# Kernel tuning notes

Hardware: AMD Instinct MI355X
Metric: run time of the kernel (lower is better)

Reference implementation:

```python
import jax, jax.numpy as jnp
import numpy as np

B, S, D, H = 4, 1024, 1024, 16
DH = D // H  # head_dim = 64


def setup_inputs() -> dict:
    key = jax.random.key(0)
    kq, kk, kv, kl, kwq, kwk, kwv, kwo = jax.random.split(key, 8)
    query = jax.random.normal(kq, (B, S, D), dtype=jnp.float32)
    key_t = jax.random.normal(kk, (B, S, D), dtype=jnp.float32)
    value = jax.random.normal(kv, (B, S, D), dtype=jnp.float32)
    # padding: keys at positions >= valid length are padded (True)
    lengths = jax.random.randint(kl, (B,), S // 2, S + 1)
    key_padding_mask = jnp.arange(S)[None, :] >= lengths[:, None]  # [B,S] bool
    scale = 1.0 / np.sqrt(D)
    Wq = jax.random.normal(kwq, (D, D), dtype=jnp.float32) * scale
    Wk = jax.random.normal(kwk, (D, D), dtype=jnp.float32) * scale
    Wv = jax.random.normal(kwv, (D, D), dtype=jnp.float32) * scale
    Wo = jax.random.normal(kwo, (D, D), dtype=jnp.float32) * scale
    gamma = jnp.ones((H,), dtype=jnp.float32)
    return {"query": query, "key": key_t, "value": value,
            "key_padding_mask": key_padding_mask,
            "Wq": Wq, "Wk": Wk, "Wv": Wv, "Wo": Wo, "gamma": gamma}


def reference(query, key, value, key_padding_mask, Wq, Wk, Wv, Wo, gamma):
    # nn.Linear(x) = x @ W.T (bias=False)
    q = jnp.einsum('bsd,ed->bse', query, Wq).reshape(B, S, H, DH).transpose(0, 2, 1, 3)  # [B,H,S,Dh]
    k = jnp.einsum('bsd,ed->bse', key, Wk).reshape(B, S, H, DH).transpose(0, 2, 1, 3)
    v = jnp.einsum('bsd,ed->bse', value, Wv).reshape(B, S, H, DH).transpose(0, 2, 1, 3)
    scores = jnp.einsum('bhqd,bhkd->bhqk', q, k) / jnp.sqrt(jnp.float32(DH))
    pad = key_padding_mask[:, None, None, :]  # [B,1,1,S]
    scores = jnp.where(pad, -jnp.inf, scores)
    v = jnp.where(key_padding_mask[:, None, :, None], 0.0, v)
    attn = jax.nn.softmax(scores, axis=-1)  # dropout p=0 (eval) -> identity
    ws = jnp.einsum('bhqk,bhkd->bhqd', attn, v)
    ws = ws * gamma[None, :, None, None]  # per-head scale
    ws = ws.transpose(0, 2, 1, 3).reshape(B, S, D)
    return jnp.einsum('bsd,ed->bse', ws, Wo)
```

## Files before the change

### kernel.cpp

```cpp
#include <hip/hip_runtime.h>
#include <math.h>

#define S_LEN 1024
#define DMODEL 1024

typedef __attribute__((ext_vector_type(8))) short bf16x8;
typedef __attribute__((ext_vector_type(4))) short bf16x4;
typedef __attribute__((ext_vector_type(4))) float f32x4;

#define MFMA16(a, b, c) __builtin_amdgcn_mfma_f32_16x16x32_bf16(a, b, c, 0, 0, 0)

#define WP (1024u * 1024u)
#define XP (4u * 1024u * 1024u)

__device__ __forceinline__ unsigned short rne_bf16(float f) {
    unsigned u = __float_as_uint(f);
    u += 0x7FFFu + ((u >> 16) & 1u);
    return (unsigned short)(u >> 16);
}

__device__ __forceinline__ void split_rne(float f, unsigned short& h, unsigned short& l) {
    unsigned short hh = rne_bf16(f);
    float lf = f - __uint_as_float(((unsigned)hh) << 16);
    h = hh;
    l = rne_bf16(lf);
}

typedef const __attribute__((address_space(1))) unsigned int* gas_t;
typedef __attribute__((address_space(3))) unsigned int* las_t;
__device__ __forceinline__ void glds16(const void* g, void* l) {
    __builtin_amdgcn_global_load_lds((gas_t)g, (las_t)l, 16, 0, 0);
}

__global__ __launch_bounds__(256)
void convert_wx(const float* __restrict__ W0, const float* __restrict__ W1,
                const float* __restrict__ W2, const float* __restrict__ W3,
                const float* __restrict__ Xq, const float* __restrict__ Xk,
                const float* __restrict__ Xv,
                unsigned short* __restrict__ Wpl, unsigned short* __restrict__ Xbase) {
    int blk = blockIdx.x;
    if (blk < 4096) {
        const int which = blk >> 10;
        const float* W = which == 0 ? W0 : which == 1 ? W1 : which == 2 ? W2 : W3;
        int i = ((blk & 1023) * 256 + threadIdx.x) * 4;
        float4 f = *(const float4*)&W[i];
        if (which == 3) {
            unsigned short* hi = Wpl + 3 * WP;
            unsigned short* lo = Wpl + 4 * WP;
            bf16x4 h, l;
            unsigned short hh, ll;
            split_rne(f.x, hh, ll); h[0] = (short)hh; l[0] = (short)ll;
            split_rne(f.y, hh, ll); h[1] = (short)hh; l[1] = (short)ll;
            split_rne(f.z, hh, ll); h[2] = (short)hh; l[2] = (short)ll;
            split_rne(f.w, hh, ll); h[3] = (short)hh; l[3] = (short)ll;
            *(bf16x4*)&hi[i] = h;
            *(bf16x4*)&lo[i] = l;
        } else {
            unsigned short* hi = Wpl + (size_t)which * WP;
            bf16x4 h;
            h[0] = (short)rne_bf16(f.x);
            h[1] = (short)rne_bf16(f.y);
            h[2] = (short)rne_bf16(f.z);
            h[3] = (short)rne_bf16(f.w);
            *(bf16x4*)&hi[i] = h;
        }
    } else {
        blk -= 4096;
        const int which = blk >> 12;
        const float* X = which == 0 ? Xq : which == 1 ? Xk : Xv;
        unsigned short* Xr = Xbase + (size_t)which * XP;
        int i = ((blk & 4095) * 256 + threadIdx.x) * 4;
        float4 f = *(const float4*)&X[i];
        bf16x4 h;
        h[0] = (short)rne_bf16(f.x);
        h[1] = (short)rne_bf16(f.y);
        h[2] = (short)rne_bf16(f.z);
        h[3] = (short)rne_bf16(f.w);
        *(bf16x4*)&Xr[i] = h;
    }
}

__global__ __launch_bounds__(256)
void gemm_proj(const unsigned short* __restrict__ Xbase,
               const unsigned short* __restrict__ Wpl,
               unsigned short* __restrict__ Obase) {
    __shared__ unsigned short AS[128 * 32];
    __shared__ unsigned short BS[128 * 32];

    const int z = blockIdx.z;
    const unsigned short* A = Xbase + (size_t)z * XP;
    const unsigned short* B = Wpl + (size_t)z * WP;

    const int t = threadIdx.x, lane = t & 63, w = t >> 6;
    const int quad = lane >> 4, l15 = lane & 15;
    const int wr = w & 1, wc = w >> 1;

    const int linb = blockIdx.x + (blockIdx.y << 3);
    const int swz = ((linb & 7) << 5) + (linb >> 3);
    const int bx = swz & 7, by = swz >> 3;
    const int rowBase = by * 128, colBase = bx * 128;

    const unsigned short* gA[2];
    const unsigned short* gB[2];
    unsigned short* lA[2];
    unsigned short* lB[2];
    #pragma unroll
    for (int e = 0; e < 2; e++) {
        int row = w * 32 + e * 16 + (lane >> 2);
        int cg = (lane & 3) ^ ((row >> 1) & 3);
        gA[e] = A + (size_t)(rowBase + row) * 1024 + cg * 8;
        gB[e] = B + (size_t)(colBase + row) * 1024 + cg * 8;
        lA[e] = &AS[(w * 32 + e * 16) * 32];
        lB[e] = &BS[(w * 32 + e * 16) * 32];
    }

    int aAd[4], bAd[4];
    #pragma unroll
    for (int i = 0; i < 4; i++) {
        int ra = wr * 64 + i * 16 + l15;
        aAd[i] = ra * 32 + (quad ^ ((ra >> 1) & 3)) * 8;
        int rb = wc * 64 + i * 16 + l15;
        bAd[i] = rb * 32 + (quad ^ ((rb >> 1) & 3)) * 8;
    }

    f32x4 acc[4][4] = {};

    for (int kt = 0; kt < 32; kt++) {
        if (kt) __syncthreads();
        const int ko = kt * 32;
        glds16(gA[0] + ko, lA[0]);
        glds16(gA[1] + ko, lA[1]);
        glds16(gB[0] + ko, lB[0]);
        glds16(gB[1] + ko, lB[1]);
        __syncthreads();

        bf16x8 af[4], bfr[4];
        #pragma unroll
        for (int i = 0; i < 4; i++) af[i] = *(const bf16x8*)&AS[aAd[i]];
        #pragma unroll
        for (int j = 0; j < 4; j++) bfr[j] = *(const bf16x8*)&BS[bAd[j]];
        #pragma unroll
        for (int j = 0; j < 4; j++)
            #pragma unroll
            for (int i = 0; i < 4; i++)
                acc[i][j] = MFMA16(af[i], bfr[j], acc[i][j]);
    }

    unsigned short* O = Obase + (size_t)z * XP;
    #pragma unroll
    for (int i = 0; i < 4; i++)
        #pragma unroll
        for (int j = 0; j < 4; j++)
            #pragma unroll
            for (int r = 0; r < 4; r++) {
                int m = rowBase + wr * 64 + i * 16 + quad * 4 + r;
                int n = colBase + wc * 64 + j * 16 + l15;
                int bb = m >> 10, s = m & 1023, hh = n >> 6, dh = n & 63;
                size_t hb = ((size_t)(bb * 16 + hh)) << 16;
                unsigned short v = rne_bf16(acc[i][j][r]);
                if (z == 2) O[hb + (size_t)dh * 1024 + s] = v;
                else        O[hb + s * 64 + dh] = v;
            }
}

__global__ __launch_bounds__(256)
void gemm_out2(const unsigned short* __restrict__ A,
               const unsigned short* __restrict__ Bh, const unsigned short* __restrict__ Bl,
               float* __restrict__ Cf) {
    __shared__ unsigned short AS[128 * 32];
    __shared__ unsigned short BhS[64 * 32], BlS[64 * 32];

    const int t = threadIdx.x, lane = t & 63, w = t >> 6;
    const int quad = lane >> 4, l15 = lane & 15;
    const int wr = w & 1, wc = w >> 1;

    const int linb = blockIdx.x + (blockIdx.y << 4);
    const int swz = ((linb & 7) << 6) + (linb >> 3);
    const int bx = swz & 15, by = swz >> 4;
    const int rowBase = by * 128, colBase = bx * 64;

    const unsigned short* gA[2];
    unsigned short* lA[2];
    #pragma unroll
    for (int e = 0; e < 2; e++) {
        int row = w * 32 + e * 16 + (lane >> 2);
        int cg = (lane & 3) ^ ((row >> 1) & 3);
        gA[e] = A + (size_t)(rowBase + row) * 1024 + cg * 8;
        lA[e] = &AS[(w * 32 + e * 16) * 32];
    }
    const unsigned short *gBh, *gBl;
    unsigned short *lBh, *lBl;
    {
        int row = w * 16 + (lane >> 2);
        int cg = (lane & 3) ^ ((row >> 1) & 3);
        gBh = Bh + (size_t)(colBase + row) * 1024 + cg * 8;
        gBl = Bl + (size_t)(colBase + row) * 1024 + cg * 8;
        lBh = &BhS[(w * 16) * 32];
        lBl = &BlS[(w * 16) * 32];
    }

    int aAd[4], bAd[2];
    #pragma unroll
    for (int i = 0; i < 4; i++) {
        int ra = wr * 64 + i * 16 + l15;
        aAd[i] = ra * 32 + (quad ^ ((ra >> 1) & 3)) * 8;
    }
    #pragma unroll
    for (int j = 0; j < 2; j++) {
        int rb = wc * 32 + j * 16 + l15;
        bAd[j] = rb * 32 + (quad ^ ((rb >> 1) & 3)) * 8;
    }

    f32x4 acc[4][2] = {};

    for (int kt = 0; kt < 32; kt++) {
        if (kt) __syncthreads();
        const int ko = kt * 32;
        glds16(gA[0] + ko, lA[0]);
        glds16(gA[1] + ko, lA[1]);
        glds16(gBh + ko, lBh);
        glds16(gBl + ko, lBl);
        __syncthreads();

        bf16x8 af[4], bhf[2], blf[2];
        #pragma unroll
        for (int i = 0; i < 4; i++) af[i] = *(const bf16x8*)&AS[aAd[i]];
        #pragma unroll
        for (int j = 0; j < 2; j++) {
            bhf[j] = *(const bf16x8*)&BhS[bAd[j]];
            blf[j] = *(const bf16x8*)&BlS[bAd[j]];
        }
        #pragma unroll
        for (int j = 0; j < 2; j++)
            #pragma unroll
            for (int i = 0; i < 4; i++) {
                acc[i][j] = MFMA16(af[i], bhf[j], acc[i][j]);
                acc[i][j] = MFMA16(af[i], blf[j], acc[i][j]);
            }
    }

    #pragma unroll
    for (int i = 0; i < 4; i++)
        #pragma unroll
        for (int j = 0; j < 2; j++)
            #pragma unroll
            for (int r = 0; r < 4; r++) {
                int m = rowBase + wr * 64 + i * 16 + quad * 4 + r;
                int n = colBase + wc * 32 + j * 16 + l15;
                Cf[(size_t)m * 1024 + n] = acc[i][j][r];
            }
}

__global__ __launch_bounds__(256)
void attn_mfma(const unsigned short* __restrict__ Qr, const unsigned short* __restrict__ Kr,
               const unsigned short* __restrict__ Vt,
               const int* __restrict__ mask, const float* __restrict__ gamma,
               unsigned short* __restrict__ WSr) {
    __shared__ int maskS[1024];
    __shared__ unsigned short Ks[64 * 72];
    __shared__ unsigned short Vs[64 * 72];
    __shared__ unsigned short Ph[4 * 16 * 72];

    const int t = threadIdx.x, lane = t & 63, w = t >> 6;
    const int quad = lane >> 4, l15 = lane & 15;

    const int linb = blockIdx.x + (blockIdx.y << 4);
    const int swz = ((linb & 7) << 5) + (linb >> 3);
    const int qx = swz & 15, h = swz >> 4;

    const int q0 = qx * 64, b = blockIdx.z;
    const size_t hb = ((size_t)(b * 16 + h)) << 16;

    ((int4*)maskS)[t] = ((const int4*)(mask + b * 1024))[t];

    bf16x8 qhi[2];
    {
        const int qrow = q0 + w * 16 + l15;
        const size_t qb = hb + (size_t)qrow * 64 + quad * 8;
        qhi[0] = *(const bf16x8*)&Qr[qb];
        qhi[1] = *(const bf16x8*)&Qr[qb + 32];
    }

    f32x4 o[4] = {};
    float lsum[4] = {0.f, 0.f, 0.f, 0.f};

    __syncthreads();

    for (int jt = 0; jt < 16; jt++) {
        const int j0 = jt * 64;
        if (maskS[j0]) break;
        const bool partial = maskS[j0 + 63] != 0;
        __syncthreads();
        #pragma unroll
        for (int e = 0; e < 2; e++) {
            int lin = e * 256 + t;
            int c = lin & 7, row = lin >> 3;
            *(bf16x8*)&Ks[row * 72 + c * 8] =
                *(const bf16x8*)&Kr[hb + (size_t)(j0 + row) * 64 + c * 8];
            *(bf16x8*)&Vs[row * 72 + c * 8] =
                *(const bf16x8*)&Vt[hb + (size_t)row * 1024 + j0 + c * 8];
        }
        __syncthreads();

        f32x4 s4[4] = {};
        #pragma unroll
        for (int nj = 0; nj < 4; nj++) {
            int kr = (nj * 16 + l15) * 72 + quad * 8;
            #pragma unroll
            for (int kk = 0; kk < 2; kk++) {
                bf16x8 kv = *(const bf16x8*)&Ks[kr + kk * 32];
                s4[nj] = MFMA16(qhi[kk], kv, s4[nj]);
            }
        }

        if (partial) {
            #pragma unroll
            for (int nj = 0; nj < 4; nj++) {
                int mk = maskS[j0 + nj * 16 + l15];
                #pragma unroll
                for (int r = 0; r < 4; r++) {
                    float p = mk ? 0.f : __expf(s4[nj][r] * 0.125f);
                    lsum[r] += p;
                    Ph[(w * 16 + quad * 4 + r) * 72 + nj * 16 + l15] = rne_bf16(p);
                }
            }
        } else {
            #pragma unroll
            for (int nj = 0; nj < 4; nj++) {
                #pragma unroll
                for (int r = 0; r < 4; r++) {
                    float p = __expf(s4[nj][r] * 0.125f);
                    lsum[r] += p;
                    Ph[(w * 16 + quad * 4 + r) * 72 + nj * 16 + l15] = rne_bf16(p);
                }
            }
        }

        bf16x8 ph[2];
        #pragma unroll
        for (int ks = 0; ks < 2; ks++)
            ph[ks] = *(const bf16x8*)&Ph[(w * 16 + l15) * 72 + ks * 32 + quad * 8];
        #pragma unroll
        for (int dt = 0; dt < 4; dt++) {
            int vr = (dt * 16 + l15) * 72 + quad * 8;
            #pragma unroll
            for (int ks = 0; ks < 2; ks++) {
                bf16x8 vv = *(const bf16x8*)&Vs[vr + ks * 32];
                o[dt] = MFMA16(ph[ks], vv, o[dt]);
            }
        }
    }

    #pragma unroll
    for (int r = 0; r < 4; r++) {
        lsum[r] += __shfl_xor(lsum[r], 1);
        lsum[r] += __shfl_xor(lsum[r], 2);
        lsum[r] += __shfl_xor(lsum[r], 4);
        lsum[r] += __shfl_xor(lsum[r], 8);
    }

    const float g = gamma[h];
    #pragma unroll
    for (int r = 0; r < 4; r++) {
        const int qrow = q0 + w * 16 + quad * 4 + r;
        const float sc = g / lsum[r];
        const size_t base = ((size_t)b * 1024 + qrow) * 1024 + h * 64;
        #pragma unroll
        for (int dt = 0; dt < 4; dt++)
            WSr[base + dt * 16 + l15] = rne_bf16(o[dt][r] * sc);
    }
}

extern "C" void kernel_launch(void* const* d_in, const int* in_sizes, int n_in,
                              void* d_out, int out_size, void* d_ws, size_t ws_size,
                              hipStream_t stream) {
    const float* query = (const float*)d_in[0];
    const float* key   = (const float*)d_in[1];
    const float* value = (const float*)d_in[2];
    const int*   mask  = (const int*)d_in[3];
    const float* Wq    = (const float*)d_in[4];
    const float* Wk    = (const float*)d_in[5];
    const float* Wv    = (const float*)d_in[6];
    const float* Wo    = (const float*)d_in[7];
    const float* gamma = (const float*)d_in[8];
    float* out = (float*)d_out;

    unsigned short* u = (unsigned short*)d_ws;
    unsigned short* Xbase = u;
    unsigned short* Obase = u + 3 * XP;
    unsigned short* Wpl   = u + 6 * XP;
    unsigned short* WSr   = Xbase;
    unsigned short* Qr = Obase, *Kr = Obase + XP, *Vt = Obase + 2 * XP;
    unsigned short* Woh = Wpl + 3 * WP, *Wol = Wpl + 4 * WP;

    convert_wx<<<16384, 256, 0, stream>>>(Wq, Wk, Wv, Wo, query, key, value, Wpl, Xbase);

    gemm_proj<<<dim3(8, 32, 3), 256, 0, stream>>>(Xbase, Wpl, Obase);

    attn_mfma<<<dim3(16, 16, 4), 256, 0, stream>>>(Qr, Kr, Vt, mask, gamma, WSr);

    gemm_out2<<<dim3(16, 32), 256, 0, stream>>>(WSr, Woh, Wol, out);
}
```

Before: 208.4 us.

## Rewrite QKV projection GEMM as 256x256 tile, 8-wave double-buffered pipeline

The projection GEMM changes from 128x128 tiles with a single LDS buffer and full sync per K-step to 256x256 tiles with 512 threads. LDS is double-buffered with BK=64, and global-to-LDS loads are interleaved with the MFMA phases using explicit waitcnt/barrier scheduling, setprio, and a new XOR swizzle. The block index is also remapped for L2 locality across the three projections. The goal is more data reuse per tile and hiding load latency behind MFMAs. The cost is heavy LDS use (128KB), higher register pressure, and only 192 blocks, which may underfill the CUs.

```diff
diff --git a/kernel.cpp b/kernel.cpp
--- a/kernel.cpp
+++ b/kernel.cpp
@@ -80,81 +80,138 @@
     }
 }
 
-__global__ __launch_bounds__(256)
+__global__ __launch_bounds__(512, 2)
 void gemm_proj(const unsigned short* __restrict__ Xbase,
                const unsigned short* __restrict__ Wpl,
                unsigned short* __restrict__ Obase) {
-    __shared__ unsigned short AS[128 * 32];
-    __shared__ unsigned short BS[128 * 32];
-
-    const int z = blockIdx.z;
+    __shared__ unsigned short As[2][2][128 * 64];
+    __shared__ unsigned short Bs[2][2][128 * 64];
+
+    const int t = threadIdx.x, lane = t & 63, w = t >> 6;
+    const int quad = lane >> 4, l15 = lane & 15;
+    const int wm = w >> 2, wn = w & 3;
+
+    const int g = blockIdx.z * 64 + blockIdx.y * 4 + blockIdx.x;
+    const int sg = (g & 7) * 24 + (g >> 3);
+    const int z = sg >> 6, rem = sg & 63;
+    const int rowBase = (rem >> 2) * 256, colBase = (rem & 3) * 256;
+
     const unsigned short* A = Xbase + (size_t)z * XP;
     const unsigned short* B = Wpl + (size_t)z * WP;
 
-    const int t = threadIdx.x, lane = t & 63, w = t >> 6;
-    const int quad = lane >> 4, l15 = lane & 15;
-    const int wr = w & 1, wc = w >> 1;
-
-    const int linb = blockIdx.x + (blockIdx.y << 3);
-    const int swz = ((linb & 7) << 5) + (linb >> 3);
-    const int bx = swz & 7, by = swz >> 3;
-    const int rowBase = by * 128, colBase = bx * 128;
-
-    const unsigned short* gA[2];
-    const unsigned short* gB[2];
-    unsigned short* lA[2];
-    unsigned short* lB[2];
-    #pragma unroll
-    for (int e = 0; e < 2; e++) {
-        int row = w * 32 + e * 16 + (lane >> 2);
-        int cg = (lane & 3) ^ ((row >> 1) & 3);
-        gA[e] = A + (size_t)(rowBase + row) * 1024 + cg * 8;
-        gB[e] = B + (size_t)(colBase + row) * 1024 + cg * 8;
-        lA[e] = &AS[(w * 32 + e * 16) * 32];
-        lB[e] = &BS[(w * 32 + e * 16) * 32];
-    }
-
-    int aAd[4], bAd[4];
-    #pragma unroll
-    for (int i = 0; i < 4; i++) {
-        int ra = wr * 64 + i * 16 + l15;
-        aAd[i] = ra * 32 + (quad ^ ((ra >> 1) & 3)) * 8;
-        int rb = wc * 64 + i * 16 + l15;
-        bAd[i] = rb * 32 + (quad ^ ((rb >> 1) & 3)) * 8;
-    }
-
-    f32x4 acc[4][4] = {};
-
-    for (int kt = 0; kt < 32; kt++) {
-        if (kt) __syncthreads();
-        const int ko = kt * 32;
-        glds16(gA[0] + ko, lA[0]);
-        glds16(gA[1] + ko, lA[1]);
-        glds16(gB[0] + ko, lB[0]);
-        glds16(gB[1] + ko, lB[1]);
-        __syncthreads();
-
-        bf16x8 af[4], bfr[4];
-        #pragma unroll
-        for (int i = 0; i < 4; i++) af[i] = *(const bf16x8*)&AS[aAd[i]];
-        #pragma unroll
-        for (int j = 0; j < 4; j++) bfr[j] = *(const bf16x8*)&BS[bAd[j]];
+    const unsigned short* gAs[2][2];
+    const unsigned short* gBs[2][2];
+    #pragma unroll
+    for (int h = 0; h < 2; h++)
+        #pragma unroll
+        for (int r = 0; r < 2; r++) {
+            int lrow = r * 64 + w * 8 + (lane >> 3);
+            int cg = (lane & 7) ^ (lrow & 7);
+            gAs[h][r] = A + (size_t)(rowBase + h * 128 + lrow) * 1024 + cg * 8;
+            gBs[h][r] = B + (size_t)(colBase + h * 128 + lrow) * 1024 + cg * 8;
+        }
+    const int ld0 = (w * 8) * 64, ld1 = (64 + w * 8) * 64;
+
+    int aOff[8][2], bOff[4][2];
+    #pragma unroll
+    for (int i = 0; i < 8; i++)
+        #pragma unroll
+        for (int kk = 0; kk < 2; kk++) {
+            int lr = i * 16 + l15;
+            aOff[i][kk] = lr * 64 + (((quad + kk * 4) ^ (lr & 7)) << 3);
+        }
+    #pragma unroll
+    for (int j = 0; j < 4; j++)
+        #pragma unroll
+        for (int kk = 0; kk < 2; kk++) {
+            int lr = (wn & 1) * 64 + j * 16 + l15;
+            bOff[j][kk] = lr * 64 + (((quad + kk * 4) ^ (lr & 7)) << 3);
+        }
+
+    f32x4 acc[8][4] = {};
+
+    glds16(gAs[0][0], &As[0][0][ld0]);
+    glds16(gAs[0][1], &As[0][0][ld1]);
+    glds16(gAs[1][0], &As[0][1][ld0]);
+    glds16(gAs[1][1], &As[0][1][ld1]);
+    glds16(gBs[0][0], &Bs[0][0][ld0]);
+    glds16(gBs[0][1], &Bs[0][0][ld1]);
+    glds16(gBs[1][0], &Bs[0][1][ld0]);
+    glds16(gBs[1][1], &Bs[0][1][ld1]);
+    glds16(gBs[0][0] + 64, &Bs[1][0][ld0]);
+    glds16(gBs[0][1] + 64, &Bs[1][0][ld1]);
+    glds16(gBs[1][0] + 64, &Bs[1][1][ld0]);
+    glds16(gBs[1][1] + 64, &Bs[1][1][ld1]);
+    asm volatile("s_waitcnt vmcnt(4)" ::: "memory");
+    __builtin_amdgcn_sched_barrier(0);
+    __builtin_amdgcn_s_barrier();
+
+    for (int kt = 0; kt < 16; kt++) {
+        const int buf = kt & 1;
+        const unsigned short* Ab = As[buf][wm];
+        const unsigned short* Bb = Bs[buf][wn >> 1];
+        bf16x8 bfr[4][2];
+        #pragma unroll
+        for (int p = 0; p < 4; p++) {
+            bf16x8 af[2][2];
+            #pragma unroll
+            for (int ii = 0; ii < 2; ii++)
+                #pragma unroll
+                for (int kk = 0; kk < 2; kk++)
+                    af[ii][kk] = *(const bf16x8*)&Ab[aOff[2 * p + ii][kk]];
+            if (p == 0) {
+                #pragma unroll
+                for (int j = 0; j < 4; j++)
+                    #pragma unroll
+                    for (int kk = 0; kk < 2; kk++)
+                        bfr[j][kk] = *(const bf16x8*)&Bb[bOff[j][kk]];
+            }
+            if (p == 0 && kt + 1 < 16) {
+                glds16(gAs[0][0] + (kt + 1) * 64, &As[buf ^ 1][0][ld0]);
+                glds16(gAs[0][1] + (kt + 1) * 64, &As[buf ^ 1][0][ld1]);
+            }
+            if (p == 1 && kt + 1 < 16) {
+                glds16(gAs[1][0] + (kt + 1) * 64, &As[buf ^ 1][1][ld0]);
+                glds16(gAs[1][1] + (kt + 1) * 64, &As[buf ^ 1][1][ld1]);
+            }
+            if (p == 2 && kt + 2 < 16) {
+                glds16(gBs[0][0] + (kt + 2) * 64, &Bs[buf][0][ld0]);
+                glds16(gBs[0][1] + (kt + 2) * 64, &Bs[buf][0][ld1]);
+            }
+            if (p == 3 && kt + 2 < 16) {
+                glds16(gBs[1][0] + (kt + 2) * 64, &Bs[buf][1][ld0]);
+                glds16(gBs[1][1] + (kt + 2) * 64, &Bs[buf][1][ld1]);
+            }
+            __builtin_amdgcn_s_barrier();
+            asm volatile("s_waitcnt lgkmcnt(0)" ::: "memory");
+            __builtin_amdgcn_sched_barrier(0);
+            __builtin_amdgcn_s_setprio(1);
+            #pragma unroll
+            for (int ii = 0; ii < 2; ii++)
+                #pragma unroll
+                for (int j = 0; j < 4; j++)
+                    #pragma unroll
+                    for (int kk = 0; kk < 2; kk++)
+                        acc[2 * p + ii][j] = MFMA16(af[ii][kk], bfr[j][kk], acc[2 * p + ii][j]);
+            __builtin_amdgcn_s_setprio(0);
+            if (p == 3) {
+                if (kt < 14) asm volatile("s_waitcnt vmcnt(4)" ::: "memory");
+                else         asm volatile("s_waitcnt vmcnt(0)" ::: "memory");
+                __builtin_amdgcn_sched_barrier(0);
+            }
+            __builtin_amdgcn_s_barrier();
+        }
+    }
+
+    unsigned short* O = Obase + (size_t)z * XP;
+    #pragma unroll
+    for (int i = 0; i < 8; i++)
         #pragma unroll
         for (int j = 0; j < 4; j++)
             #pragma unroll
-            for (int i = 0; i < 4; i++)
-                acc[i][j] = MFMA16(af[i], bfr[j], acc[i][j]);
-    }
-
-    unsigned short* O = Obase + (size_t)z * XP;
-    #pragma unroll
-    for (int i = 0; i < 4; i++)
-        #pragma unroll
-        for (int j = 0; j < 4; j++)
-            #pragma unroll
             for (int r = 0; r < 4; r++) {
-                int m = rowBase + wr * 64 + i * 16 + quad * 4 + r;
-                int n = colBase + wc * 64 + j * 16 + l15;
+                int m = rowBase + wm * 128 + i * 16 + quad * 4 + r;
+                int n = colBase + wn * 64 + j * 16 + l15;
                 int bb = m >> 10, s = m & 1023, hh = n >> 6, dh = n & 63;
                 size_t hb = ((size_t)(bb * 16 + hh)) << 16;
                 unsigned short v = rne_bf16(acc[i][j][r]);
@@ -395,7 +452,7 @@
 
     convert_wx<<<16384, 256, 0, stream>>>(Wq, Wk, Wv, Wo, query, key, value, Wpl, Xbase);
 
-    gemm_proj<<<dim3(8, 32, 3), 256, 0, stream>>>(Xbase, Wpl, Obase);
+    gemm_proj<<<dim3(4, 16, 3), 512, 0, stream>>>(Xbase, Wpl, Obase);
 
     attn_mfma<<<dim3(16, 16, 4), 256, 0, stream>>>(Qr, Kr, Vt, mask, gamma, WSr);
 
```

Result: slower. 233.1 us (+11.8%).

## Prefetch next K/V tile into registers during attention compute and raise MFMA priority

Applied to the files above, without the earlier changes.

The attention loop now loads the next 64-key K and V tile from global memory into registers while the current tile's QK and PV MFMAs run. It stores that tile to shared memory at the end of each iteration, so global-load latency is hidden instead of exposed between barriers. It also wraps the MFMA blocks in s_setprio to favour matrix issue. This costs extra registers and a more complex barrier structure, and the attention kernel may be only part of total time.

```diff
diff --git a/kernel.cpp b/kernel.cpp
--- a/kernel.cpp
+++ b/kernel.cpp
@@ -281,28 +281,46 @@
         qhi[1] = *(const bf16x8*)&Qr[qb + 32];
     }
 
+    const int sc = (t & 7) * 8;
+    const int sr = t >> 3;
+
     f32x4 o[4] = {};
     float lsum[4] = {0.f, 0.f, 0.f, 0.f};
 
+    bf16x8 kreg[2], vreg[2];
+    #pragma unroll
+    for (int e = 0; e < 2; e++) {
+        int row = e * 32 + sr;
+        kreg[e] = *(const bf16x8*)&Kr[hb + (size_t)row * 64 + sc];
+        vreg[e] = *(const bf16x8*)&Vt[hb + (size_t)row * 1024 + sc];
+    }
+    __syncthreads();
+    #pragma unroll
+    for (int e = 0; e < 2; e++) {
+        int row = e * 32 + sr;
+        *(bf16x8*)&Ks[row * 72 + sc] = kreg[e];
+        *(bf16x8*)&Vs[row * 72 + sc] = vreg[e];
+    }
     __syncthreads();
 
     for (int jt = 0; jt < 16; jt++) {
         const int j0 = jt * 64;
         if (maskS[j0]) break;
         const bool partial = maskS[j0 + 63] != 0;
-        __syncthreads();
-        #pragma unroll
-        for (int e = 0; e < 2; e++) {
-            int lin = e * 256 + t;
-            int c = lin & 7, row = lin >> 3;
-            *(bf16x8*)&Ks[row * 72 + c * 8] =
-                *(const bf16x8*)&Kr[hb + (size_t)(j0 + row) * 64 + c * 8];
-            *(bf16x8*)&Vs[row * 72 + c * 8] =
-                *(const bf16x8*)&Vt[hb + (size_t)row * 1024 + j0 + c * 8];
-        }
-        __syncthreads();
+        const int j0n = j0 + 64;
+        const bool pf = (jt < 15) && (maskS[j0n] == 0);
+
+        if (pf) {
+            #pragma unroll
+            for (int e = 0; e < 2; e++) {
+                int row = e * 32 + sr;
+                kreg[e] = *(const bf16x8*)&Kr[hb + (size_t)(j0n + row) * 64 + sc];
+                vreg[e] = *(const bf16x8*)&Vt[hb + (size_t)row * 1024 + j0n + sc];
+            }
+        }
 
         f32x4 s4[4] = {};
+        __builtin_amdgcn_s_setprio(1);
         #pragma unroll
         for (int nj = 0; nj < 4; nj++) {
             int kr = (nj * 16 + l15) * 72 + quad * 8;
@@ -312,6 +330,7 @@
                 s4[nj] = MFMA16(qhi[kk], kv, s4[nj]);
             }
         }
+        __builtin_amdgcn_s_setprio(0);
 
         if (partial) {
             #pragma unroll
@@ -340,6 +359,7 @@
         #pragma unroll
         for (int ks = 0; ks < 2; ks++)
             ph[ks] = *(const bf16x8*)&Ph[(w * 16 + l15) * 72 + ks * 32 + quad * 8];
+        __builtin_amdgcn_s_setprio(1);
         #pragma unroll
         for (int dt = 0; dt < 4; dt++) {
             int vr = (dt * 16 + l15) * 72 + quad * 8;
@@ -348,6 +368,18 @@
                 bf16x8 vv = *(const bf16x8*)&Vs[vr + ks * 32];
                 o[dt] = MFMA16(ph[ks], vv, o[dt]);
             }
+        }
+        __builtin_amdgcn_s_setprio(0);
+
+        if (pf) {
+            __syncthreads();
+            #pragma unroll
+            for (int e = 0; e < 2; e++) {
+                int row = e * 32 + sr;
+                *(bf16x8*)&Ks[row * 72 + sc] = kreg[e];
+                *(bf16x8*)&Vs[row * 72 + sc] = vreg[e];
+            }
+            __syncthreads();
         }
     }
 
@@ -363,11 +395,11 @@
     #pragma unroll
     for (int r = 0; r < 4; r++) {
         const int qrow = q0 + w * 16 + quad * 4 + r;
-        const float sc = g / lsum[r];
+        const float sc2 = g / lsum[r];
         const size_t base = ((size_t)b * 1024 + qrow) * 1024 + h * 64;
         #pragma unroll
         for (int dt = 0; dt < 4; dt++)
-            WSr[base + dt * 16 + l15] = rne_bf16(o[dt][r] * sc);
+            WSr[base + dt * 16 + l15] = rne_bf16(o[dt][r] * sc2);
     }
 }
 
```

Measured after the change: 209.1 us. About the same (+0.3%).
